# Optimization experiments

Hardware: AMD Instinct MI355X
Metric: run time of the kernel (lower is better)

## Reference

```python
import jax, jax.numpy as jnp
import numpy as np

DIM = 128
NH = 4
K = 7
PAD = K // 2  # dilation = 1
MLP_HID = 4 * DIM
EPS = 1e-5


def _layernorm(x, w, b):
    m = jnp.mean(x, axis=-1, keepdims=True)
    v = jnp.mean((x - m) ** 2, axis=-1, keepdims=True)
    return (x - m) / jnp.sqrt(v + EPS) * w + b


def _windows(xp, H, W):
    # xp: [B, nh, Hp, Wp, hd] zero-padded; returns [B, nh, H, W, hd, K*K]
    return jnp.stack(
        [xp[:, :, i:i + H, j:j + W, :] for i in range(K) for j in range(K)],
        axis=-1,
    )


def setup_inputs() -> dict:
    key = jax.random.key(0)
    ks = jax.random.split(key, 10)
    s = 0.02
    inp = {
        "x": jax.random.normal(ks[0], (4, 56, 56, DIM), dtype=jnp.float32),
        "ln1_w": jnp.ones((DIM,), jnp.float32),
        "ln1_b": jnp.zeros((DIM,), jnp.float32),
        "w_qkv": jax.random.normal(ks[1], (DIM, 3 * DIM), jnp.float32) * s,
        "b_qkv": jnp.zeros((3 * DIM,), jnp.float32),
        "rpb": jax.random.normal(ks[2], (NH, K * K), jnp.float32) * s,
        "w_proj": jax.random.normal(ks[3], (DIM, DIM), jnp.float32) * s,
        "b_proj": jnp.zeros((DIM,), jnp.float32),
        "ln2_w": jnp.ones((DIM,), jnp.float32),
        "ln2_b": jnp.zeros((DIM,), jnp.float32),
        "w_fc1": jax.random.normal(ks[4], (DIM, MLP_HID), jnp.float32) * s,
        "b_fc1": jnp.zeros((MLP_HID,), jnp.float32),
        "w_fc2": jax.random.normal(ks[5], (MLP_HID, DIM), jnp.float32) * s,
        "b_fc2": jnp.zeros((DIM,), jnp.float32),
    }
    return inp


def _nat_block(x, ln1_w, ln1_b, w_qkv, b_qkv, rpb, w_proj, b_proj,
               ln2_w, ln2_b, w_fc1, b_fc1, w_fc2, b_fc2):
    B, H, W, C = x.shape
    hd = C // NH
    scale = hd ** -0.5

    # --- neighborhood attention ---
    xn = _layernorm(x, ln1_w, ln1_b)
    qkv = xn @ w_qkv + b_qkv                       # [B,H,W,3C]
    qkv = qkv.reshape(B, H, W, 3, NH, hd)
    qkv = jnp.transpose(qkv, (3, 0, 4, 1, 2, 5))   # [3,B,nh,H,W,hd]
    q, k, v = qkv[0] * scale, qkv[1], qkv[2]
    # zero-pad spatial dims (matches F.pad with constant 0 in original)
    pad = ((0, 0), (0, 0), (PAD, PAD), (PAD, PAD), (0, 0))
    kp = jnp.pad(k, pad)
    vp = jnp.pad(v, pad)
    kw = _windows(kp, H, W)                        # [B,nh,H,W,hd,49]
    vw = _windows(vp, H, W)
    attn = jnp.einsum('bnhwd,bnhwdk->bnhwk', q, kw)
    attn = attn + rpb[None, :, None, None, :]
    attn = jax.nn.softmax(attn, axis=-1)
    out = jnp.einsum('bnhwk,bnhwdk->bnhwd', attn, vw)  # [B,nh,H,W,hd]
    out = jnp.transpose(out, (0, 2, 3, 1, 4)).reshape(B, H, W, C)
    x = x + (out @ w_proj + b_proj)

    # --- MLP ---
    xn2 = _layernorm(x, ln2_w, ln2_b)
    h = jax.nn.gelu(xn2 @ w_fc1 + b_fc1, approximate=False)
    x = x + (h @ w_fc2 + b_fc2)
    return x


def reference(x, ln1_w, ln1_b, w_qkv, b_qkv, rpb, w_proj, b_proj,
              ln2_w, ln2_b, w_fc1, b_fc1, w_fc2, b_fc2):
    return _nat_block(x, ln1_w, ln1_b, w_qkv, b_qkv, rpb, w_proj, b_proj,
                      ln2_w, ln2_b, w_fc1, b_fc1, w_fc2, b_fc2)
```

## Files before the change

kernel.cpp:

```cpp
#include <hip/hip_runtime.h>

using bf16x8 = __attribute__((ext_vector_type(8))) short;
using f32x4  = __attribute__((ext_vector_type(4))) float;
typedef unsigned short u16;
typedef __attribute__((ext_vector_type(8))) unsigned short u16x8;
typedef __attribute__((ext_vector_type(4))) unsigned short u16x4;

__device__ __forceinline__ u16 f2b(float f){
  unsigned int i=__float_as_uint(f);
  return (u16)((i + 0x7FFFu + ((i>>16)&1u))>>16);
}
__device__ __forceinline__ float b2f(u16 u){
  union{unsigned int i; float f;}v; v.i=((unsigned int)u)<<16; return v.f;
}
__device__ __forceinline__ void async16(const void* g, void* l){
  __builtin_amdgcn_global_load_lds((__attribute__((address_space(1))) void*)(g),
                                   (__attribute__((address_space(3))) void*)(l), 16, 0, 0);
}
__device__ __forceinline__ float gelu_tanh(float v){
  float u = v*(0.7978845608f + 0.0356774081f*v*v);
  float e = __expf(-2.0f*fabsf(u));
  float th = (1.0f-e)/(1.0f+e);
  th = (u<0.f)? -th : th;
  return 0.5f*v*(1.0f+th);
}

#define BARX() do{ __asm__ volatile("" ::: "memory"); \
                   __builtin_amdgcn_s_barrier(); \
                   __asm__ volatile("" ::: "memory"); }while(0)
#define WAITV(n) __asm__ volatile("s_waitcnt vmcnt(" #n ")" ::: "memory")
#define WAITL()  __asm__ volatile("s_waitcnt lgkmcnt(0)" ::: "memory")

__global__ void prep_kernel(const float* __restrict__ wqkv, const float* __restrict__ wproj,
                            const float* __restrict__ wfc1, const float* __restrict__ wfc2,
                            u16* __restrict__ tqkv, u16* __restrict__ tproj,
                            u16* __restrict__ tfc1, u16* __restrict__ tfc2)
{
  int idx = blockIdx.x*256 + threadIdx.x;
  if (idx < 49152){
    int nc = idx>>14, r = idx&16383, i = r>>3, e = r&7, n = i&127, c = i>>7;
    tqkv[idx] = f2b(wqkv[(c*8+e)*384 + nc*128 + n]);
  } else if (idx < 65536){
    int r = idx-49152; int i=r>>3, e=r&7, n=i&127, c=i>>7;
    tproj[r] = f2b(wproj[(c*8+e)*128 + n]);
  } else if (idx < 131072){
    int t = idx-65536; int nc=t>>14, r=t&16383, i=r>>3, e=r&7, n=i&127, c=i>>7;
    tfc1[t] = f2b(wfc1[(c*8+e)*512 + nc*128 + n]);
  } else if (idx < 196608){
    int t = idx-131072; int nc=t>>14, r=t&16383, i=r>>3, e=r&7, n=i&127, c=i>>7;
    tfc2[t] = f2b(wfc2[(nc*128 + c*8 + e)*128 + n]);
  }
}


__global__ __launch_bounds__(256)
void qkv_ln_kernel(const float* __restrict__ x,
                   const float* __restrict__ ln1w, const float* __restrict__ ln1b,
                   const u16* __restrict__ tqkv, const float* __restrict__ bqkv,
                   u16* __restrict__ qb, u16* __restrict__ kb, u16* __restrict__ vb)
{
  __shared__ __align__(16) char smem[40960];
  char* lA = smem;
  char* lB = smem + 8192;

  const int tid = threadIdx.x;
  const int lane = tid&63, wid = tid>>6;
  const int quad = lane>>4, lrow = lane&15;
  const int m0 = blockIdx.x*32;
  const int nc = blockIdx.y;
  const int wm = (wid&1)*16, wn = (wid>>1)*64;

  #pragma unroll
  for (int kk=0;kk<8;kk++){
    int i = tid + kk*256;
    async16(tqkv + (size_t)nc*16384 + i*8, lB + i*16);
  }

  {
    const int row = tid>>3, g = tid&7;
    float xv[16];
    const float4* xr = (const float4*)(x + (size_t)(m0+row)*128 + g*16);
    float s=0.f, sq=0.f;
    #pragma unroll
    for (int c4=0;c4<4;c4++){
      float4 t = xr[c4];
      xv[c4*4]=t.x; xv[c4*4+1]=t.y; xv[c4*4+2]=t.z; xv[c4*4+3]=t.w;
      s += t.x+t.y+t.z+t.w;
      sq += t.x*t.x+t.y*t.y+t.z*t.z+t.w*t.w;
    }
    s  += __shfl_xor(s,1);  s  += __shfl_xor(s,2);  s  += __shfl_xor(s,4);
    sq += __shfl_xor(sq,1); sq += __shfl_xor(sq,2); sq += __shfl_xor(sq,4);
    float mean = s*0.0078125f;
    float rstd = rsqrtf(sq*0.0078125f - mean*mean + 1e-5f);
    const float4* wr = (const float4*)(ln1w + g*16);
    const float4* br = (const float4*)(ln1b + g*16);
    u16 nv[16];
    #pragma unroll
    for (int c4=0;c4<4;c4++){
      float4 w4 = wr[c4], b4 = br[c4];
      nv[c4*4]   = f2b((xv[c4*4]  -mean)*rstd*w4.x + b4.x);
      nv[c4*4+1] = f2b((xv[c4*4+1]-mean)*rstd*w4.y + b4.y);
      nv[c4*4+2] = f2b((xv[c4*4+2]-mean)*rstd*w4.z + b4.z);
      nv[c4*4+3] = f2b((xv[c4*4+3]-mean)*rstd*w4.w + b4.w);
    }
    #pragma unroll
    for (int cc=0;cc<2;cc++){
      u16x8 pk;
      #pragma unroll
      for (int e=0;e<8;e++) pk[e] = nv[cc*8+e];
      *(u16x8*)(lA + (((g*2+cc)*32 + row)<<4)) = pk;
    }
  }
  __syncthreads();

  f32x4 acc[4] = {};
  #pragma unroll
  for (int ks=0;ks<4;ks++){
    bf16x8 af = ((const bf16x8*)lA)[(ks*4+quad)*32 + wm + lrow];
    #pragma unroll
    for (int j=0;j<4;j++){
      bf16x8 bfr = ((const bf16x8*)lB)[(ks*4+quad)*128 + wn + j*16 + lrow];
      acc[j] = __builtin_amdgcn_mfma_f32_16x16x32_bf16(af, bfr, acc[j], 0,0,0);
    }
  }

  const float scale = 0.17677669529663687f;
  u16* dst = (nc==0)? qb : ((nc==1)? kb : vb);
  #pragma unroll
  for (int j=0;j<4;j++){
    int col = wn + j*16 + lrow;
    float bia = bqkv[nc*128 + col];
    #pragma unroll
    for (int r=0;r<4;r++){
      int row = m0 + wm + quad*4 + r;
      float val = acc[j][r] + bia;
      if (nc==0) val *= scale;
      dst[(size_t)row*128 + col] = f2b(val);
    }
  }
}

#define KT_S 40
#define VT_S 232
#define P_S  152
__global__ __launch_bounds__(256)
void attn_kernel(const u16* __restrict__ qb, const u16* __restrict__ kb,
                 const u16* __restrict__ vb, const float* __restrict__ rpb,
                 u16* __restrict__ aout)
{
  __shared__ __align__(16) char smem[50192];
  u16*  kt   = (u16*)smem;
  u16*  vt   = (u16*)(smem + 15680);
  u16*  Pm   = (u16*)(smem + 30528);
  float* srpb= (float*)(smem + 49984);

  const int tid = threadIdx.x;
  const int tile = blockIdx.x, bh = blockIdx.y;
  const int b = bh>>2, h = bh&3;
  const int ty = (tile/7)*8, tx = (tile%7)*8;
  const int lane = tid&63, wid = tid>>6;
  const int quad = lane>>4, lrow = lane&15;

  #pragma unroll
  for (int kk=0;kk<4;kk++){
    int i = tid + kk*256;
    if (i < 784){
      int pos = i>>2, oct = i&3;
      int hy = pos/14, hx = pos - hy*14;
      int gy = ty + hy - 3, gx = tx + hx - 3;
      u16x8 kv = {0,0,0,0,0,0,0,0};
      if (gy>=0 && gy<56 && gx>=0 && gx<56)
        kv = *(const u16x8*)(kb + ((size_t)(b*3136 + gy*56 + gx)*128 + h*32 + oct*8));
      *(u16x8*)(kt + pos*KT_S + oct*8) = kv;
    }
  }
  #pragma unroll
  for (int kk=0;kk<4;kk++){
    int i = tid + kk*256;
    if (i < 896){
      int pos = i>>2, oct = i&3;
      u16x8 vv = {0,0,0,0,0,0,0,0};
      if (pos < 196){
        int hy = pos/14, hx = pos - hy*14;
        int gy = ty + hy - 3, gx = tx + hx - 3;
        if (gy>=0 && gy<56 && gx>=0 && gx<56)
          vv = *(const u16x8*)(vb + ((size_t)(b*3136 + gy*56 + gx)*128 + h*32 + oct*8));
      }
      #pragma unroll
      for (int j=0;j<8;j++) vt[(oct*8+j)*VT_S + pos] = vv[j];
    }
  }
  if (tid < 49) srpb[tid] = rpb[h*49 + tid];
  __syncthreads();

  const int pxq = wid*16 + lrow;
  const int tokq = b*3136 + (ty + (pxq>>3))*56 + tx + (pxq&7);
  bf16x8 qf = *(const bf16x8*)(qb + (size_t)tokq*128 + h*32 + quad*8);

  f32x4 sc[7];
  const f32x4 zf = {0.f,0.f,0.f,0.f};
  #pragma unroll
  for (int cg=0;cg<7;cg++){
    int pos = wid*28 + cg*16 + lrow;
    bf16x8 kf = *(const bf16x8*)(kt + pos*KT_S + quad*8);
    sc[cg] = __builtin_amdgcn_mfma_f32_16x16x32_bf16(qf, kf, zf, 0,0,0);
  }

  const int lyq = quad>>1;
  #pragma unroll
  for (int cg=0;cg<7;cg++){
    int np = cg*16 + lrow;
    int nh = np/14, hx = np - nh*14;
    int dy = nh - lyq;
    #pragma unroll
    for (int r=0;r<4;r++){
      int lx = (quad*4+r)&7;
      int dx = hx - lx;
      bool in = ((unsigned)dy<7u) && ((unsigned)dx<7u);
      float bias = srpb[in ? (dy*7+dx) : 0];
      sc[cg][r] = in ? (sc[cg][r] + bias) : -1e30f;
    }
  }
  float inv[4];
  #pragma unroll
  for (int r=0;r<4;r++){
    float m = sc[0][r];
    #pragma unroll
    for (int cg=1;cg<7;cg++) m = fmaxf(m, sc[cg][r]);
    m = fmaxf(m, __shfl_xor(m,1)); m = fmaxf(m, __shfl_xor(m,2));
    m = fmaxf(m, __shfl_xor(m,4)); m = fmaxf(m, __shfl_xor(m,8));
    float l = 0.f;
    #pragma unroll
    for (int cg=0;cg<7;cg++){ float p = __expf(sc[cg][r]-m); sc[cg][r]=p; l+=p; }
    l += __shfl_xor(l,1); l += __shfl_xor(l,2);
    l += __shfl_xor(l,4); l += __shfl_xor(l,8);
    inv[r]=1.f/l;
  }

  u16* Pw = Pm + wid*16*P_S;
  #pragma unroll
  for (int cg=0;cg<7;cg++){
    int np = cg*16 + lrow;
    #pragma unroll
    for (int r=0;r<4;r++)
      Pw[(quad*4+r)*P_S + np] = f2b(sc[cg][r]);
  }
  { int zr = lane>>2, seg = lane&3;
    u16x4 z4 = {0,0,0,0};
    *(u16x4*)(Pw + zr*P_S + 112 + seg*4) = z4; }
  __syncthreads();

  f32x4 oacc[2] = {zf, zf};
  #pragma unroll
  for (int ks=0;ks<4;ks++){
    bf16x8 pf = *(const bf16x8*)(Pw + lrow*P_S + ks*32 + quad*8);
    #pragma unroll
    for (int cg2=0;cg2<2;cg2++){
      bf16x8 vf = *(const bf16x8*)(vt + (cg2*16+lrow)*VT_S + wid*28 + ks*32 + quad*8);
      oacc[cg2] = __builtin_amdgcn_mfma_f32_16x16x32_bf16(pf, vf, oacc[cg2], 0,0,0);
    }
  }
  #pragma unroll
  for (int r=0;r<4;r++){
    int px = wid*16 + quad*4 + r;
    int tok = b*3136 + (ty + (px>>3))*56 + tx + (px&7);
    #pragma unroll
    for (int cg2=0;cg2<2;cg2++){
      int ch = h*32 + cg2*16 + lrow;
      aout[(size_t)((tok>>5)*16 + (ch>>3))*256 + (tok&31)*8 + (ch&7)]
        = f2b(oacc[cg2][r]*inv[r]);
    }
  }
}


__device__ __forceinline__ void stage32k(const u16* __restrict__ src, char* dst, int tid){
  #pragma unroll
  for (int kk=0;kk<4;kk++){ int i = tid + kk*512; async16(src + (size_t)i*8, dst + i*16); }
}

__device__ __forceinline__ void mfma16(const char* Ab, const char* Bb,
                                       int quad, int lrow, int wm, int wn, f32x4 acc[4]){
  const int row = wm + lrow;
  #pragma unroll
  for (int ks=0;ks<4;ks++){
    bf16x8 af = ((const bf16x8*)Ab)[(row>>5)*512 + (ks*4+quad)*32 + (row&31)];
    #pragma unroll
    for (int j=0;j<4;j++){
      bf16x8 bfr = ((const bf16x8*)Bb)[(ks*4+quad)*128 + wn + j*16 + lrow];
      acc[j] = __builtin_amdgcn_mfma_f32_16x16x32_bf16(af, bfr, acc[j], 0,0,0);
    }
  }
}

__device__ __forceinline__ void fc1_phase(const char* xn2, const char* B, char* lA,
                                          const float* __restrict__ bfc1c,
                                          int quad, int lrow, int wm, int wn){
  f32x4 a2[4] = {};
  __builtin_amdgcn_s_setprio(1);
  mfma16(xn2, B, quad, lrow, wm, wn, a2);
  __builtin_amdgcn_s_setprio(0);
  #pragma unroll
  for (int j=0;j<4;j++){
    int col = wn + j*16 + lrow;
    float bia = bfc1c[col];
    #pragma unroll
    for (int r=0;r<4;r++){
      int row = wm + quad*4 + r;
      float g = gelu_tanh(a2[j][r] + bia);
      ((u16*)lA)[(row>>5)*4096 + ((col>>3)*32 + (row&31))*8 + (col&7)] = f2b(g);
    }
  }
}

__global__ __launch_bounds__(512)
void mega_mlp_kernel(const u16* __restrict__ aout, const float* __restrict__ x,
                     const u16* __restrict__ tproj, const float* __restrict__ bproj,
                     const float* __restrict__ ln2w, const float* __restrict__ ln2b,
                     const u16* __restrict__ tfc1, const float* __restrict__ bfc1,
                     const u16* __restrict__ tfc2, const float* __restrict__ bfc2,
                     float* __restrict__ out)
{
  __shared__ __align__(16) char smem[131072];
  char* B0  = smem;
  char* B1  = smem + 32768;
  char* B2  = smem + 65536;
  char* lA  = smem + 98304;
  char* xn2 = smem + 114688;
  float* redS = (float*)lA;
  float* redQ = redS + 128;

  const int tid = threadIdx.x;
  const int lane = tid&63, wid = tid>>6;
  const int quad = lane>>4, lrow = lane&15;
  const int m0 = blockIdx.x*64;
  const int wm = (wid&3)*16, wn = (wid>>2)*64;
  const int half = wid>>2;

  float xv[4][4];
  #pragma unroll
  for (int j=0;j<4;j++){
    #pragma unroll
    for (int r=0;r<4;r++)
      xv[j][r] = x[(size_t)(m0+wm+quad*4+r)*128 + wn + j*16 + lrow];
  }

  stage32k(tproj, B0, tid);
  #pragma unroll
  for (int kk=0;kk<2;kk++){
    int i = tid + kk*512;
    async16(aout + (size_t)blockIdx.x*8192 + i*8, lA + i*16);
  }
  stage32k(tfc1,           B1, tid);
  stage32k(tfc2,           B2, tid);
  WAITV(8); BARX();

  f32x4 acc[4] = {};
  __builtin_amdgcn_s_setprio(1);
  mfma16(lA, B0, quad, lrow, wm, wn, acc);
  __builtin_amdgcn_s_setprio(0);
  float x1v[4][4]; float ps[4]={0,0,0,0}, pq[4]={0,0,0,0};
  #pragma unroll
  for (int j=0;j<4;j++){
    float bia = bproj[wn + j*16 + lrow];
    #pragma unroll
    for (int r=0;r<4;r++){
      float val = acc[j][r] + bia + xv[j][r];
      x1v[j][r] = val; ps[r]+=val; pq[r]+=val*val;
    }
  }
  #pragma unroll
  for (int r=0;r<4;r++){
    #pragma unroll
    for (int off=1; off<16; off<<=1){
      ps[r]+=__shfl_xor(ps[r],off); pq[r]+=__shfl_xor(pq[r],off);
    }
  }
  BARX();
  stage32k(tfc1 + 16384,   B0, tid);
  if (lrow==0){
    #pragma unroll
    for (int r=0;r<4;r++){
      int row = wm + quad*4 + r;
      redS[half*64+row]=ps[r]; redQ[half*64+row]=pq[r];
    }
  }
  WAITL(); WAITV(8); BARX();

  {
    float w2[4], b2[4];
    #pragma unroll
    for (int j=0;j<4;j++){ int col=wn+j*16+lrow; w2[j]=ln2w[col]; b2[j]=ln2b[col]; }
    #pragma unroll
    for (int r=0;r<4;r++){
      int row = wm + quad*4 + r;
      float mean = (redS[row]+redS[64+row])*0.0078125f;
      float var  = (redQ[row]+redQ[64+row])*0.0078125f - mean*mean;
      float rstd = rsqrtf(var + 1e-5f);
      #pragma unroll
      for (int j=0;j<4;j++){
        int col = wn + j*16 + lrow;
        ((u16*)xn2)[(row>>5)*4096 + ((col>>3)*32 + (row&31))*8 + (col&7)]
          = f2b((x1v[j][r]-mean)*rstd*w2[j] + b2[j]);
      }
    }
  }
  WAITL(); BARX();

  f32x4 acc3[4] = {};

  fc1_phase(xn2, B1, lA, bfc1, quad, lrow, wm, wn);
  WAITL(); BARX();
  stage32k(tfc2 + 16384,   B1, tid);
  WAITV(8); BARX();

  __builtin_amdgcn_s_setprio(1);
  mfma16(lA, B2, quad, lrow, wm, wn, acc3);
  __builtin_amdgcn_s_setprio(0);
  BARX();
  stage32k(tfc1 + 2*16384, B2, tid);
  WAITV(8); BARX();

  fc1_phase(xn2, B0, lA, bfc1 + 128, quad, lrow, wm, wn);
  WAITL(); BARX();
  stage32k(tfc2 + 2*16384, B0, tid);
  WAITV(8); BARX();

  __builtin_amdgcn_s_setprio(1);
  mfma16(lA, B1, quad, lrow, wm, wn, acc3);
  __builtin_amdgcn_s_setprio(0);
  BARX();
  stage32k(tfc1 + 3*16384, B1, tid);
  WAITV(8); BARX();

  fc1_phase(xn2, B2, lA, bfc1 + 256, quad, lrow, wm, wn);
  WAITL(); BARX();
  stage32k(tfc2 + 3*16384, B2, tid);
  WAITV(8); BARX();

  __builtin_amdgcn_s_setprio(1);
  mfma16(lA, B0, quad, lrow, wm, wn, acc3);
  __builtin_amdgcn_s_setprio(0);
  WAITV(4); BARX();

  fc1_phase(xn2, B1, lA, bfc1 + 384, quad, lrow, wm, wn);
  WAITL(); WAITV(0); BARX();

  __builtin_amdgcn_s_setprio(1);
  mfma16(lA, B2, quad, lrow, wm, wn, acc3);
  __builtin_amdgcn_s_setprio(0);

  #pragma unroll
  for (int j=0;j<4;j++){
    int col = wn + j*16 + lrow;
    float bia = bfc2[col];
    #pragma unroll
    for (int r=0;r<4;r++){
      int row = m0 + wm + quad*4 + r;
      out[(size_t)row*128 + col] = acc3[j][r] + bia + x1v[j][r];
    }
  }
}

extern "C" void kernel_launch(void* const* d_in, const int* in_sizes, int n_in,
                              void* d_out, int out_size, void* d_ws, size_t ws_size,
                              hipStream_t stream)
{
  const float* x     =(const float*)d_in[0];
  const float* ln1w  =(const float*)d_in[1];
  const float* ln1b  =(const float*)d_in[2];
  const float* wqkv  =(const float*)d_in[3];
  const float* bqkv  =(const float*)d_in[4];
  const float* rpb   =(const float*)d_in[5];
  const float* wproj =(const float*)d_in[6];
  const float* bproj =(const float*)d_in[7];
  const float* ln2w  =(const float*)d_in[8];
  const float* ln2b  =(const float*)d_in[9];
  const float* wfc1  =(const float*)d_in[10];
  const float* bfc1  =(const float*)d_in[11];
  const float* wfc2  =(const float*)d_in[12];
  const float* bfc2  =(const float*)d_in[13];

  char* ws=(char*)d_ws;
  size_t o=0;
  u16* tqkv =(u16*)(ws+o); o+=98304;
  u16* tproj=(u16*)(ws+o); o+=32768;
  u16* tfc1 =(u16*)(ws+o); o+=131072;
  u16* tfc2 =(u16*)(ws+o); o+=131072;
  u16* aout =(u16*)(ws+o); o+=3211264;
  u16* qb   =(u16*)(ws+o); o+=3211264;
  u16* kb   =(u16*)(ws+o); o+=3211264;
  u16* vb   =(u16*)(ws+o); o+=3211264;

  prep_kernel<<<768,256,0,stream>>>(wqkv,wproj,wfc1,wfc2,tqkv,tproj,tfc1,tfc2);
  qkv_ln_kernel<<<dim3(392,3),256,0,stream>>>(x,ln1w,ln1b,tqkv,bqkv,qb,kb,vb);
  attn_kernel<<<dim3(49,16),256,0,stream>>>(qb,kb,vb,rpb,aout);
  mega_mlp_kernel<<<196,512,0,stream>>>(aout,x,tproj,bproj,ln2w,ln2b,
                                        tfc1,bfc1,tfc2,bfc2,(float*)d_out);
}
```

Measured before the change: 128.3 us.

## Remove prep kernel: convert QKV weights in-kernel, fold MLP weight prep into attention

Drops the separate weight-conversion launch. The QKV kernel now reads fp32 weights directly, converts them to bf16 in LDS, and loops over q/k/v in one block using double-buffered LDS, so each block normalizes x only once. Conversion of the projection and MLP weights moves into the first 576 blocks of the attention kernel. This saves one launch and the redundant layernorm work, but each of the 392 QKV blocks now re-reads and converts the full QKV weight matrix, and its LDS use grows to 72KB, which can lower occupancy.

```diff
diff --git a/kernel.cpp b/kernel.cpp
--- a/kernel.cpp
+++ b/kernel.cpp
@@ -31,59 +31,64 @@
 #define WAITV(n) __asm__ volatile("s_waitcnt vmcnt(" #n ")" ::: "memory")
 #define WAITL()  __asm__ volatile("s_waitcnt lgkmcnt(0)" ::: "memory")
 
-__global__ void prep_kernel(const float* __restrict__ wqkv, const float* __restrict__ wproj,
-                            const float* __restrict__ wfc1, const float* __restrict__ wfc2,
-                            u16* __restrict__ tqkv, u16* __restrict__ tproj,
-                            u16* __restrict__ tfc1, u16* __restrict__ tfc2)
-{
-  int idx = blockIdx.x*256 + threadIdx.x;
-  if (idx < 49152){
-    int nc = idx>>14, r = idx&16383, i = r>>3, e = r&7, n = i&127, c = i>>7;
-    tqkv[idx] = f2b(wqkv[(c*8+e)*384 + nc*128 + n]);
-  } else if (idx < 65536){
-    int r = idx-49152; int i=r>>3, e=r&7, n=i&127, c=i>>7;
-    tproj[r] = f2b(wproj[(c*8+e)*128 + n]);
-  } else if (idx < 131072){
-    int t = idx-65536; int nc=t>>14, r=t&16383, i=r>>3, e=r&7, n=i&127, c=i>>7;
-    tfc1[t] = f2b(wfc1[(c*8+e)*512 + nc*128 + n]);
-  } else if (idx < 196608){
-    int t = idx-131072; int nc=t>>14, r=t&16383, i=r>>3, e=r&7, n=i&127, c=i>>7;
-    tfc2[t] = f2b(wfc2[(nc*128 + c*8 + e)*128 + n]);
-  }
-}
 
 
 __global__ __launch_bounds__(256)
 void qkv_ln_kernel(const float* __restrict__ x,
                    const float* __restrict__ ln1w, const float* __restrict__ ln1b,
-                   const u16* __restrict__ tqkv, const float* __restrict__ bqkv,
+                   const float* __restrict__ wqkv, const float* __restrict__ bqkv,
                    u16* __restrict__ qb, u16* __restrict__ kb, u16* __restrict__ vb)
 {
-  __shared__ __align__(16) char smem[40960];
+  __shared__ __align__(16) char smem[73728];
   char* lA = smem;
-  char* lB = smem + 8192;
+  char* B0 = smem + 8192;
+  char* B1 = smem + 40960;
 
   const int tid = threadIdx.x;
   const int lane = tid&63, wid = tid>>6;
   const int quad = lane>>4, lrow = lane&15;
   const int m0 = blockIdx.x*32;
-  const int nc = blockIdx.y;
   const int wm = (wid&1)*16, wn = (wid>>1)*64;
 
-  #pragma unroll
-  for (int kk=0;kk<8;kk++){
-    int i = tid + kk*256;
-    async16(tqkv + (size_t)nc*16384 + i*8, lB + i*16);
-  }
-
+  const int c0u = tid>>5, c1u = (tid>>5)+8;
+  const int n0u = (tid&31)*4;
+
+  const int row8 = tid>>3, g = tid&7;
+  float4 xl[4];
   {
-    const int row = tid>>3, g = tid&7;
+    const float4* xr = (const float4*)(x + (size_t)(m0+row8)*128 + g*16);
+    #pragma unroll
+    for (int c4=0;c4<4;c4++) xl[c4] = xr[c4];
+  }
+
+  float4 wreg[2][8];
+  #define WISSUE(ncc) do{ \
+    const float* wp0 = wqkv + (size_t)(ncc)*128 + (size_t)c0u*8*384 + n0u; \
+    const float* wp1 = wqkv + (size_t)(ncc)*128 + (size_t)c1u*8*384 + n0u; \
+    _Pragma("unroll") \
+    for (int e=0;e<8;e++){ wreg[0][e] = *(const float4*)(wp0 + e*384); \
+                           wreg[1][e] = *(const float4*)(wp1 + e*384); } }while(0)
+
+  #define WCONV(Bp) do{ \
+    _Pragma("unroll") \
+    for (int uu=0;uu<2;uu++){ \
+      int base = ((uu? c1u : c0u)*128 + n0u); \
+      _Pragma("unroll") \
+      for (int d=0;d<4;d++){ \
+        u16x8 pk; \
+        _Pragma("unroll") \
+        for (int e=0;e<8;e++){ float4 t = wreg[uu][e]; \
+          pk[e] = f2b(d==0? t.x : d==1? t.y : d==2? t.z : t.w); } \
+        *(u16x8*)((Bp) + ((base+d)<<4)) = pk; } } }while(0)
+
+  WISSUE(0);
+
+  {
     float xv[16];
-    const float4* xr = (const float4*)(x + (size_t)(m0+row)*128 + g*16);
     float s=0.f, sq=0.f;
     #pragma unroll
     for (int c4=0;c4<4;c4++){
-      float4 t = xr[c4];
+      float4 t = xl[c4];
       xv[c4*4]=t.x; xv[c4*4+1]=t.y; xv[c4*4+2]=t.z; xv[c4*4+3]=t.w;
       s += t.x+t.y+t.z+t.w;
       sq += t.x*t.x+t.y*t.y+t.z*t.z+t.w*t.w;
@@ -108,36 +113,47 @@
       u16x8 pk;
       #pragma unroll
       for (int e=0;e<8;e++) pk[e] = nv[cc*8+e];
-      *(u16x8*)(lA + (((g*2+cc)*32 + row)<<4)) = pk;
-    }
-  }
-  __syncthreads();
-
-  f32x4 acc[4] = {};
-  #pragma unroll
-  for (int ks=0;ks<4;ks++){
-    bf16x8 af = ((const bf16x8*)lA)[(ks*4+quad)*32 + wm + lrow];
-    #pragma unroll
-    for (int j=0;j<4;j++){
-      bf16x8 bfr = ((const bf16x8*)lB)[(ks*4+quad)*128 + wn + j*16 + lrow];
-      acc[j] = __builtin_amdgcn_mfma_f32_16x16x32_bf16(af, bfr, acc[j], 0,0,0);
-    }
-  }
-
-  const float scale = 0.17677669529663687f;
-  u16* dst = (nc==0)? qb : ((nc==1)? kb : vb);
-  #pragma unroll
-  for (int j=0;j<4;j++){
-    int col = wn + j*16 + lrow;
-    float bia = bqkv[nc*128 + col];
-    #pragma unroll
-    for (int r=0;r<4;r++){
-      int row = m0 + wm + quad*4 + r;
-      float val = acc[j][r] + bia;
-      if (nc==0) val *= scale;
-      dst[(size_t)row*128 + col] = f2b(val);
-    }
-  }
+      *(u16x8*)(lA + (((g*2+cc)*32 + row8)<<4)) = pk;
+    }
+  }
+
+  WCONV(B0);
+  WISSUE(1);
+  WAITL(); BARX();
+
+  f32x4 acc[4];
+  #define MFMAPH(Bp) do{ \
+    _Pragma("unroll") for (int j=0;j<4;j++){ f32x4 z={0.f,0.f,0.f,0.f}; acc[j]=z; } \
+    _Pragma("unroll") \
+    for (int ks=0;ks<4;ks++){ \
+      bf16x8 af = ((const bf16x8*)lA)[(ks*4+quad)*32 + wm + lrow]; \
+      _Pragma("unroll") \
+      for (int j=0;j<4;j++){ \
+        bf16x8 bfr = ((const bf16x8*)(Bp))[(ks*4+quad)*128 + wn + j*16 + lrow]; \
+        acc[j] = __builtin_amdgcn_mfma_f32_16x16x32_bf16(af, bfr, acc[j], 0,0,0); } } }while(0)
+
+  #define QSTORE(ncc, dstp, doscale) do{ \
+    _Pragma("unroll") \
+    for (int j=0;j<4;j++){ \
+      int col = wn + j*16 + lrow; \
+      float bia = bqkv[(ncc)*128 + col]; \
+      _Pragma("unroll") \
+      for (int r=0;r<4;r++){ \
+        int row = m0 + wm + quad*4 + r; \
+        float val = acc[j][r] + bia; \
+        if (doscale) val *= 0.17677669529663687f; \
+        (dstp)[(size_t)row*128 + col] = f2b(val); } } }while(0)
+
+  MFMAPH(B0); QSTORE(0, qb, 1);
+  WCONV(B1);
+  WISSUE(2);
+  WAITL(); BARX();
+
+  MFMAPH(B1); QSTORE(1, kb, 0);
+  WCONV(B0);
+  WAITL(); BARX();
+
+  MFMAPH(B0); QSTORE(2, vb, 0);
 }
 
 #define KT_S 40
@@ -146,6 +162,9 @@
 __global__ __launch_bounds__(256)
 void attn_kernel(const u16* __restrict__ qb, const u16* __restrict__ kb,
                  const u16* __restrict__ vb, const float* __restrict__ rpb,
+                 const float* __restrict__ wproj, const float* __restrict__ wfc1,
+                 const float* __restrict__ wfc2,
+                 u16* __restrict__ tproj, u16* __restrict__ tfc1, u16* __restrict__ tfc2,
                  u16* __restrict__ aout)
 {
   __shared__ __align__(16) char smem[50192];
@@ -160,6 +179,25 @@
   const int ty = (tile/7)*8, tx = (tile%7)*8;
   const int lane = tid&63, wid = tid>>6;
   const int quad = lane>>4, lrow = lane&15;
+
+  {
+    int bid = bh*49 + tile;
+    if (bid < 576){
+      int Wd = bid*256 + tid;
+      float v; u16* dst;
+      if (Wd < 16384){
+        int i=Wd>>3, e=Wd&7, n=i&127, c=i>>7;
+        v = wproj[(c*8+e)*128 + n]; dst = tproj + Wd;
+      } else if (Wd < 81920){
+        int t = Wd - 16384; int ncc=t>>14, r=t&16383, i=r>>3, e=r&7, n=i&127, c=i>>7;
+        v = wfc1[(c*8+e)*512 + ncc*128 + n]; dst = tfc1 + t;
+      } else {
+        int t = Wd - 81920; int ncc=t>>14, r=t&16383, i=r>>3, e=r&7, n=i&127, c=i>>7;
+        v = wfc2[(ncc*128 + c*8 + e)*128 + n]; dst = tfc2 + t;
+      }
+      *dst = f2b(v);
+    }
+  }
 
   #pragma unroll
   for (int kk=0;kk<4;kk++){
@@ -272,7 +310,6 @@
     }
   }
 }
-
 
 __device__ __forceinline__ void stage32k(const u16* __restrict__ src, char* dst, int tid){
   #pragma unroll
@@ -483,7 +520,6 @@
 
   char* ws=(char*)d_ws;
   size_t o=0;
-  u16* tqkv =(u16*)(ws+o); o+=98304;
   u16* tproj=(u16*)(ws+o); o+=32768;
   u16* tfc1 =(u16*)(ws+o); o+=131072;
   u16* tfc2 =(u16*)(ws+o); o+=131072;
@@ -492,9 +528,9 @@
   u16* kb   =(u16*)(ws+o); o+=3211264;
   u16* vb   =(u16*)(ws+o); o+=3211264;
 
-  prep_kernel<<<768,256,0,stream>>>(wqkv,wproj,wfc1,wfc2,tqkv,tproj,tfc1,tfc2);
-  qkv_ln_kernel<<<dim3(392,3),256,0,stream>>>(x,ln1w,ln1b,tqkv,bqkv,qb,kb,vb);
-  attn_kernel<<<dim3(49,16),256,0,stream>>>(qb,kb,vb,rpb,aout);
+  qkv_ln_kernel<<<392,256,0,stream>>>(x,ln1w,ln1b,wqkv,bqkv,qb,kb,vb);
+  attn_kernel<<<dim3(49,16),256,0,stream>>>(qb,kb,vb,rpb,wproj,wfc1,wfc2,
+                                            tproj,tfc1,tfc2,aout);
   mega_mlp_kernel<<<196,512,0,stream>>>(aout,x,tproj,bproj,ln2w,ln2b,
                                         tfc1,bfc1,tfc2,bfc2,(float*)d_out);
 }
```

New measurement: 130.1 us. No clear change (+1.4%).
